# Kernel optimization log

Measured on AMD Instinct MI355X. Metric: run time of the kernel, lower is better.

The kernel has to match this reference:

```python
import jax, jax.numpy as jnp
import numpy as np

B, T, H, NH = 16, 2048, 1024, 16
HD = H // NH  # 64
IN0, IN1 = 256, 512  # modality input sizes needing projection; modality 2 is already H


def _ln(x, g, b, eps=1e-5):
    m = jnp.mean(x, axis=-1, keepdims=True)
    v = jnp.mean((x - m) ** 2, axis=-1, keepdims=True)
    return (x - m) / jnp.sqrt(v + eps) * g + b


def setup_inputs() -> dict:
    key = jax.random.key(0)
    ks = jax.random.split(key, 24)
    s = 0.02
    d = {
        'x0': jax.random.normal(ks[0], (B, T, IN0), jnp.float32),
        'x1': jax.random.normal(ks[1], (B, T, IN1), jnp.float32),
        'x2': jax.random.normal(ks[2], (B, T, H), jnp.float32),
        'static_context': jax.random.normal(ks[3], (B, T, H), jnp.float32),
        'Wp0': jax.random.normal(ks[4], (H, IN0), jnp.float32) * s,
        'bp0': jnp.zeros((H,), jnp.float32),
        'Wp1': jax.random.normal(ks[5], (H, IN1), jnp.float32) * s,
        'bp1': jnp.zeros((H,), jnp.float32),
        'Wq': jax.random.normal(ks[6], (H, H), jnp.float32) * s,
        'bq': jnp.zeros((H,), jnp.float32),
        'Wk': jax.random.normal(ks[7], (H, H), jnp.float32) * s,
        'bk': jnp.zeros((H,), jnp.float32),
        'Wv': jax.random.normal(ks[8], (H, H), jnp.float32) * s,
        'bv': jnp.zeros((H,), jnp.float32),
        'Wo': jax.random.normal(ks[9], (H, H), jnp.float32) * s,
        'bo': jnp.zeros((H,), jnp.float32),
        'query_token': jax.random.normal(ks[10], (H,), jnp.float32) * s,
        'g1': jnp.ones((H,), jnp.float32),
        'be1': jnp.zeros((H,), jnp.float32),
        'g2': jnp.ones((H,), jnp.float32),
        'be2': jnp.zeros((H,), jnp.float32),
        'W1': jax.random.normal(ks[11], (4 * H, H), jnp.float32) * s,
        'b1': jnp.zeros((4 * H,), jnp.float32),
        'W2': jax.random.normal(ks[12], (H, 4 * H), jnp.float32) * s,
        'b2': jnp.zeros((H,), jnp.float32),
    }
    return d


def _forward(x0, x1, x2, static_context, Wp0, bp0, Wp1, bp1, Wq, bq, Wk, bk, Wv, bv,
             Wo, bo, query_token, g1, be1, g2, be2, W1, b1, W2, b2):
    # project modalities to hidden size, stack -> [B, T, M, H]
    m0 = x0 @ Wp0.T + bp0
    m1 = x1 @ Wp1.T + bp1
    stacked = jnp.stack([m0, m1, x2], axis=2)  # [B,T,3,H]
    M = stacked.shape[2]
    # per-timestep single-query cross-attention over the M modality tokens,
    # batched over all B*T positions (equivalent to the torch per-t loop)
    q = query_token + static_context  # [B,T,H]
    Q = (q @ Wq.T + bq).reshape(B, T, NH, HD)
    K = (stacked @ Wk.T + bk).reshape(B, T, M, NH, HD)
    V = (stacked @ Wv.T + bv).reshape(B, T, M, NH, HD)
    scores = jnp.einsum('bthd,btmhd->bthm', Q, K) / jnp.sqrt(jnp.asarray(HD, Q.dtype))
    attn = jax.nn.softmax(scores, axis=-1)  # [B,T,NH,M]
    weights = attn.mean(axis=2)  # average over heads (torch default) -> [B,T,M]
    ctx = jnp.einsum('bthm,btmhd->bthd', attn, V).reshape(B, T, H)
    attn_out = ctx @ Wo.T + bo
    fused = _ln(attn_out, g1, be1)
    ff = jax.nn.gelu(fused @ W1.T + b1, approximate=False) @ W2.T + b2
    fused = _ln(fused + ff, g2, be2)
    return fused, weights


def reference(x0, x1, x2, static_context, Wp0, bp0, Wp1, bp1, Wq, bq, Wk, bk, Wv, bv,
              Wo, bo, query_token, g1, be1, g2, be2, W1, b1, W2, b2):
    return _forward(x0, x1, x2, static_context, Wp0, bp0, Wp1, bp1, Wq, bq, Wk, bk,
                    Wv, bv, Wo, bo, query_token, g1, be1, g2, be2, W1, b1, W2, b2)
```

## Files before the change

kernel.cpp:

```cpp
#include <hip/hip_runtime.h>
#include <hip/hip_bf16.h>
#include <math.h>

#define BT 32768
#define HH 1024

typedef unsigned short u16;
typedef __attribute__((ext_vector_type(4))) unsigned short u16x4;
typedef __attribute__((ext_vector_type(8))) __bf16 bf16x8;
typedef __attribute__((ext_vector_type(4))) float f32x4;

#define DEVI static __device__ __forceinline__

DEVI u16 f2bf(float f){
  unsigned u = __builtin_bit_cast(unsigned, f);
  u += 0x7FFFu + ((u >> 16) & 1u);
  return (u16)(u >> 16);
}
DEVI float bf2f(u16 h){
  unsigned u = ((unsigned)h) << 16;
  return __builtin_bit_cast(float, u);
}
DEVI void gl_lds16(const void* g, void* l){
  __builtin_amdgcn_global_load_lds((const __attribute__((address_space(1))) void*)g,
                                   (__attribute__((address_space(3))) void*)l, 16, 0, 0);
}
DEVI int swz(int row, int elem){ return elem ^ ((row & 7) << 3); }

__global__ void k_cast4(const float* __restrict__ s, u16* __restrict__ d, int n4){
  int i = blockIdx.x*blockDim.x + threadIdx.x;
  int st = gridDim.x*blockDim.x;
  for (; i < n4; i += st){
    float4 v = ((const float4*)s)[i];
    u16x4 o = { f2bf(v.x), f2bf(v.y), f2bf(v.z), f2bf(v.w) };
    ((u16x4*)d)[i] = o;
  }
}

__global__ void k_pack_x2(const float* __restrict__ s, u16* __restrict__ d, int n4){
  int i = blockIdx.x*blockDim.x + threadIdx.x;
  int st = gridDim.x*blockDim.x;
  for (; i < n4; i += st){
    int e = i*4; int t = e >> 10; int c = e & 1023;
    float4 v = *(const float4*)&s[e];
    u16x4 o = { f2bf(v.x), f2bf(v.y), f2bf(v.z), f2bf(v.w) };
    *(u16x4*)&d[(size_t)t*3072 + 2048 + c] = o;
  }
}

__global__ void k_qb(const float* __restrict__ qt, const float* __restrict__ sc,
                     u16* __restrict__ d, int n4){
  int i = blockIdx.x*blockDim.x + threadIdx.x;
  int st = gridDim.x*blockDim.x;
  for (; i < n4; i += st){
    int e = i*4; int c = e & 1023;
    float4 v = *(const float4*)&sc[e];
    float4 q = *(const float4*)&qt[c];
    u16x4 o = { f2bf(v.x+q.x), f2bf(v.y+q.y), f2bf(v.z+q.z), f2bf(v.w+q.w) };
    ((u16x4*)d)[i] = o;
  }
}

__global__ void k_copyf(const float* __restrict__ s, float* __restrict__ d, int n){
  int i = blockIdx.x*blockDim.x + threadIdx.x;
  int st = gridDim.x*blockDim.x;
  for (; i < n; i += st) d[i] = s[i];
}

__global__ __launch_bounds__(256, 3)
void k_gemm(const u16* __restrict__ A, int lda,
            const u16* __restrict__ B, int ldb, int K,
            const float* __restrict__ bias,
            u16* __restrict__ C, int ldc, int col0, int act)
{
  __shared__ u16 As[128*64];
  __shared__ u16 Bs[128*64];
  const int tid = threadIdx.x, lane = tid & 63, wid = tid >> 6;
  const int wr = wid >> 1, wc = wid & 1;
  const int r15 = lane & 15, g = lane >> 4;
  const int m0 = blockIdx.x * 128, n0 = blockIdx.y * 128;
  f32x4 acc[4][4] = {};

  for (int k0 = 0; k0 < K; k0 += 64){
    #pragma unroll
    for (int it = 0; it < 4; ++it){
      int c = it*256 + tid;
      int row = c >> 3;
      int ke = swz(row, (c & 7) * 8);
      gl_lds16(A + (size_t)(m0+row)*lda + (k0+ke), As + c*8);
      gl_lds16(B + (size_t)(n0+row)*ldb + (k0+ke), Bs + c*8);
    }
    __syncthreads();
    #pragma unroll
    for (int kk = 0; kk < 64; kk += 32){
      bf16x8 av[4], bvv[4];
      #pragma unroll
      for (int i = 0; i < 4; ++i){
        int row = wr*64 + i*16 + r15;
        av[i] = *(const bf16x8*)&As[row*64 + swz(row, kk + g*8)];
      }
      #pragma unroll
      for (int j = 0; j < 4; ++j){
        int row = wc*64 + j*16 + r15;
        bvv[j] = *(const bf16x8*)&Bs[row*64 + swz(row, kk + g*8)];
      }
      #pragma unroll
      for (int i = 0; i < 4; ++i)
        #pragma unroll
        for (int j = 0; j < 4; ++j)
          acc[i][j] = __builtin_amdgcn_mfma_f32_16x16x32_bf16(av[i], bvv[j], acc[i][j], 0, 0, 0);
    }
    __syncthreads();
  }
  #pragma unroll
  for (int j = 0; j < 4; ++j){
    int col = wc*64 + j*16 + r15;
    float bb = bias ? bias[n0 + col] : 0.f;
    #pragma unroll
    for (int i = 0; i < 4; ++i){
      #pragma unroll
      for (int jj = 0; jj < 4; ++jj){
        int row = wr*64 + i*16 + g*4 + jj;
        float v = acc[i][j][jj] + bb;
        if (act == 1) v = 0.5f * v * (1.f + erff(v * 0.70710678118654752f));
        C[(size_t)(m0+row)*ldc + col0 + n0 + col] = f2bf(v);
      }
    }
  }
}

__global__ __launch_bounds__(256, 3)
void k_attn(const u16* __restrict__ S, const u16* __restrict__ Wk, const u16* __restrict__ Wv,
            const float* __restrict__ bk, const float* __restrict__ bv,
            const u16* __restrict__ Q, u16* __restrict__ ctx, float* __restrict__ wacc)
{
  __shared__ __align__(16) char smem[45056];
  u16* As  = (u16*)smem;
  u16* Bk  = (u16*)(smem + 12288);
  u16* Bv  = (u16*)(smem + 12288 + 16384);
  u16* Vl  = (u16*)smem;
  u16* Ql  = (u16*)(smem + 24576);
  float* Sl = (float*)(smem + 24576 + 8192);

  const int tid = threadIdx.x, lane = tid & 63, wid = tid >> 6;
  const int wr = wid >> 1, wcH = wid & 1;
  const int r15 = lane & 15, g = lane >> 4;
  const int bt = blockIdx.x, bn = blockIdx.y;
  const int row0 = bt * 96, n0 = bn * 128;

  f32x4 aK[3][4] = {}; f32x4 aV[3][4] = {};

  for (int k0 = 0; k0 < 1024; k0 += 64){
    #pragma unroll
    for (int it = 0; it < 3; ++it){
      int c = it*256 + tid; int row = c >> 3;
      int ke = swz(row, (c & 7) * 8);
      gl_lds16(S + (size_t)(row0+row)*1024 + k0 + ke, As + c*8);
    }
    #pragma unroll
    for (int it = 0; it < 4; ++it){
      int c = it*256 + tid; int row = c >> 3;
      int ke = swz(row, (c & 7) * 8);
      gl_lds16(Wk + (size_t)(n0+row)*1024 + k0 + ke, Bk + c*8);
      gl_lds16(Wv + (size_t)(n0+row)*1024 + k0 + ke, Bv + c*8);
    }
    __syncthreads();
    #pragma unroll
    for (int kk = 0; kk < 64; kk += 32){
      bf16x8 av[3], b1[4], b2[4];
      #pragma unroll
      for (int i = 0; i < 3; ++i){
        int row = wr*48 + i*16 + r15;
        av[i] = *(const bf16x8*)&As[row*64 + swz(row, kk + g*8)];
      }
      #pragma unroll
      for (int j = 0; j < 4; ++j){
        int row = wcH*64 + j*16 + r15;
        b1[j] = *(const bf16x8*)&Bk[row*64 + swz(row, kk + g*8)];
        b2[j] = *(const bf16x8*)&Bv[row*64 + swz(row, kk + g*8)];
      }
      #pragma unroll
      for (int i = 0; i < 3; ++i)
        #pragma unroll
        for (int j = 0; j < 4; ++j){
          aK[i][j] = __builtin_amdgcn_mfma_f32_16x16x32_bf16(av[i], b1[j], aK[i][j], 0, 0, 0);
          aV[i][j] = __builtin_amdgcn_mfma_f32_16x16x32_bf16(av[i], b2[j], aV[i][j], 0, 0, 0);
        }
    }
    __syncthreads();
  }

  #pragma unroll
  for (int j = 0; j < 4; ++j){
    int col = wcH*64 + j*16 + r15;
    float bvv = bv[n0 + col];
    #pragma unroll
    for (int i = 0; i < 3; ++i)
      #pragma unroll
      for (int jj = 0; jj < 4; ++jj){
        int row = wr*48 + i*16 + g*4 + jj;
        Vl[row*128 + col] = f2bf(aV[i][j][jj] + bvv);
      }
  }
  #pragma unroll
  for (int it = 0; it < 4; ++it){
    int c4 = it*256 + tid;
    int tt = c4 >> 5, cc = (c4 & 31)*4;
    *(u16x4*)&Ql[tt*128 + cc] = *(const u16x4*)&Q[(size_t)(bt*32 + tt)*1024 + n0 + cc];
  }
  __syncthreads();

  float bkv[4];
  #pragma unroll
  for (int j = 0; j < 4; ++j) bkv[j] = bk[n0 + wcH*64 + j*16 + r15];
  #pragma unroll
  for (int i = 0; i < 3; ++i){
    #pragma unroll
    for (int jj = 0; jj < 4; ++jj){
      int row = wr*48 + i*16 + g*4 + jj;
      int tt = row / 3;
      float s = 0.f;
      #pragma unroll
      for (int j = 0; j < 4; ++j){
        float qv = bf2f(Ql[tt*128 + wcH*64 + j*16 + r15]);
        s += (aK[i][j][jj] + bkv[j]) * qv;
      }
      s += __shfl_xor(s, 1); s += __shfl_xor(s, 2);
      s += __shfl_xor(s, 4); s += __shfl_xor(s, 8);
      if (r15 == 0) Sl[wcH*96 + row] = s * 0.125f;
    }
  }
  __syncthreads();

  const int t0 = bt*32;
  #pragma unroll
  for (int it = 0; it < 16; ++it){
    int idx = it*256 + tid;
    int tt = idx >> 7, col = idx & 127;
    int h = col >> 6;
    float s0 = Sl[h*96 + tt*3 + 0];
    float s1 = Sl[h*96 + tt*3 + 1];
    float s2 = Sl[h*96 + tt*3 + 2];
    float mx = fmaxf(s0, fmaxf(s1, s2));
    float e0 = expf(s0-mx), e1 = expf(s1-mx), e2 = expf(s2-mx);
    float inv = 1.f/(e0+e1+e2);
    e0 *= inv; e1 *= inv; e2 *= inv;
    float c = e0*bf2f(Vl[(tt*3+0)*128 + col])
            + e1*bf2f(Vl[(tt*3+1)*128 + col])
            + e2*bf2f(Vl[(tt*3+2)*128 + col]);
    ctx[(size_t)(t0+tt)*1024 + n0 + col] = f2bf(c);
    if ((col & 63) == 0){
      atomicAdd(&wacc[(size_t)(t0+tt)*3 + 0], e0*0.0625f);
      atomicAdd(&wacc[(size_t)(t0+tt)*3 + 1], e1*0.0625f);
      atomicAdd(&wacc[(size_t)(t0+tt)*3 + 2], e2*0.0625f);
    }
  }
}

__global__ __launch_bounds__(256)
void k_ln(const u16* __restrict__ X, const u16* __restrict__ R,
          const float* __restrict__ gam, const float* __restrict__ bet,
          u16* __restrict__ outb, float* __restrict__ outf)
{
  __shared__ float rs[4], rq[4];
  const int t = blockIdx.x, tid = threadIdx.x;
  const size_t base = (size_t)t*1024 + tid*4;
  u16x4 xv = *(const u16x4*)&X[base];
  float v[4];
  #pragma unroll
  for (int i = 0; i < 4; ++i) v[i] = bf2f(xv[i]);
  if (R){
    u16x4 rv = *(const u16x4*)&R[base];
    #pragma unroll
    for (int i = 0; i < 4; ++i) v[i] += bf2f(rv[i]);
  }
  float s = v[0]+v[1]+v[2]+v[3];
  float q = v[0]*v[0]+v[1]*v[1]+v[2]*v[2]+v[3]*v[3];
  #pragma unroll
  for (int m = 1; m < 64; m <<= 1){ s += __shfl_xor(s, m); q += __shfl_xor(q, m); }
  if ((tid & 63) == 0){ rs[tid>>6] = s; rq[tid>>6] = q; }
  __syncthreads();
  s = rs[0]+rs[1]+rs[2]+rs[3];
  q = rq[0]+rq[1]+rq[2]+rq[3];
  float mean = s * (1.f/1024.f);
  float var  = q * (1.f/1024.f) - mean*mean;
  float rstd = rsqrtf(var + 1e-5f);
  int c0 = tid*4;
  if (outb){
    u16x4 o;
    #pragma unroll
    for (int i = 0; i < 4; ++i) o[i] = f2bf((v[i]-mean)*rstd*gam[c0+i] + bet[c0+i]);
    *(u16x4*)&outb[base] = o;
  } else {
    float4 o;
    o.x = (v[0]-mean)*rstd*gam[c0+0] + bet[c0+0];
    o.y = (v[1]-mean)*rstd*gam[c0+1] + bet[c0+1];
    o.z = (v[2]-mean)*rstd*gam[c0+2] + bet[c0+2];
    o.w = (v[3]-mean)*rstd*gam[c0+3] + bet[c0+3];
    *(float4*)&outf[base] = o;
  }
}

extern "C" void kernel_launch(void* const* d_in, const int* in_sizes, int n_in,
                              void* d_out, int out_size, void* d_ws, size_t ws_size,
                              hipStream_t stream)
{
  (void)in_sizes; (void)n_in; (void)out_size;
  const float* x0  = (const float*)d_in[0];
  const float* x1  = (const float*)d_in[1];
  const float* x2  = (const float*)d_in[2];
  const float* sc  = (const float*)d_in[3];
  const float* Wp0 = (const float*)d_in[4];  const float* bp0 = (const float*)d_in[5];
  const float* Wp1 = (const float*)d_in[6];  const float* bp1 = (const float*)d_in[7];
  const float* Wq  = (const float*)d_in[8];  const float* bq  = (const float*)d_in[9];
  const float* Wk  = (const float*)d_in[10]; const float* bk  = (const float*)d_in[11];
  const float* Wv  = (const float*)d_in[12]; const float* bv  = (const float*)d_in[13];
  const float* Wo  = (const float*)d_in[14]; const float* bo  = (const float*)d_in[15];
  const float* qt  = (const float*)d_in[16];
  const float* g1  = (const float*)d_in[17]; const float* be1 = (const float*)d_in[18];
  const float* g2  = (const float*)d_in[19]; const float* be2 = (const float*)d_in[20];
  const float* W1  = (const float*)d_in[21]; const float* b1  = (const float*)d_in[22];
  const float* W2  = (const float*)d_in[23]; const float* b2  = (const float*)d_in[24];

  char* ws = (char*)d_ws;
  size_t off = 0;
  auto alloc = [&](size_t b)->char*{ char* p = ws + off; off += (b + 255) & ~(size_t)255; return p; };

  u16* Wp0b = (u16*)alloc((size_t)1024*256*2);
  u16* Wp1b = (u16*)alloc((size_t)1024*512*2);
  u16* Wqb  = (u16*)alloc((size_t)1024*1024*2);
  u16* Wkb  = (u16*)alloc((size_t)1024*1024*2);
  u16* Wvb  = (u16*)alloc((size_t)1024*1024*2);
  u16* Wob  = (u16*)alloc((size_t)1024*1024*2);
  u16* W1b  = (u16*)alloc((size_t)4096*1024*2);
  u16* W2b  = (u16*)alloc((size_t)1024*4096*2);
  char* stackedR = alloc((size_t)3*BT*1024*2);
  char* regA = alloc((size_t)BT*1024*2);
  char* regB = alloc((size_t)BT*1024*2);
  float* wacc = (float*)alloc((size_t)BT*3*4);
  if (off > ws_size) return;

  u16* stackedb = (u16*)stackedR;
  u16* ff1c = (u16*)stackedR;
  u16* x0b = (u16*)regA;
  u16* x1b = (u16*)(regA + (size_t)BT*256*2);
  u16* Qb  = (u16*)regA;
  u16* aob = (u16*)regA;
  u16* ff2b = (u16*)regA;
  u16* qb  = (u16*)regB;
  u16* ctxb = (u16*)regB;
  u16* f1b = (u16*)regB;

  hipMemsetAsync(wacc, 0, (size_t)BT*3*4, stream);

  dim3 B256(256);
  auto cast4 = [&](const float* s, u16* d, int n){
    k_cast4<<<dim3(1024), B256, 0, stream>>>(s, d, n >> 2);
  };
  cast4(Wp0, Wp0b, 1024*256); cast4(Wp1, Wp1b, 1024*512);
  cast4(Wq, Wqb, 1024*1024);  cast4(Wk, Wkb, 1024*1024);
  cast4(Wv, Wvb, 1024*1024);  cast4(Wo, Wob, 1024*1024);
  cast4(W1, W1b, 4096*1024);  cast4(W2, W2b, 4096*1024);
  cast4(x0, x0b, BT*256);     cast4(x1, x1b, BT*512);
  k_pack_x2<<<dim3(2048), B256, 0, stream>>>(x2, stackedb, BT*256);
  k_qb<<<dim3(2048), B256, 0, stream>>>(qt, sc, qb, BT*256);

  k_gemm<<<dim3(BT/128, 8), B256, 0, stream>>>(x0b, 256, Wp0b, 256, 256, bp0, stackedb, 3072, 0,    0);
  k_gemm<<<dim3(BT/128, 8), B256, 0, stream>>>(x1b, 512, Wp1b, 512, 512, bp1, stackedb, 3072, 1024, 0);
  k_gemm<<<dim3(BT/128, 8), B256, 0, stream>>>(qb, 1024, Wqb, 1024, 1024, bq, Qb, 1024, 0, 0);
  k_attn<<<dim3(BT/32, 8), B256, 0, stream>>>(stackedb, Wkb, Wvb, bk, bv, Qb, ctxb, wacc);
  k_gemm<<<dim3(BT/128, 8), B256, 0, stream>>>(ctxb, 1024, Wob, 1024, 1024, bo, aob, 1024, 0, 0);
  k_ln<<<dim3(BT), B256, 0, stream>>>(aob, nullptr, g1, be1, f1b, nullptr);

  for (int c = 0; c < 4; ++c){
    const u16* fa = f1b + (size_t)c*8192*1024;
    k_gemm<<<dim3(64, 32), B256, 0, stream>>>(fa, 1024, W1b, 1024, 1024, b1, ff1c, 4096, 0, 1);
    k_gemm<<<dim3(64, 8),  B256, 0, stream>>>(ff1c, 4096, W2b, 4096, 4096, b2,
                                              ff2b + (size_t)c*8192*1024, 1024, 0, 0);
  }
  float* outf = (float*)d_out;
  k_ln<<<dim3(BT), B256, 0, stream>>>(ff2b, f1b, g2, be2, nullptr, outf);
  k_copyf<<<dim3(384), B256, 0, stream>>>(wacc, outf + (size_t)BT*1024, BT*3);
}
```

Measured before the change: 1.704 ms.

## Use 256x256 double-buffered GEMM tiles with 512 threads and reorder attention grid

Replaces the 128x128 single-buffered GEMM with a 256x256 tile kernel using 8 waves, double-buffered LDS and prefetch of the next K-slice issued before computing the current one, with MFMA sections raised to higher priority. The goal is more data reuse per LDS load and overlap of global loads with matrix math. The attention launch grid is transposed so that blocks sharing the same row tile are scheduled adjacently, which should improve cache reuse of the stacked activations. In exchange, the larger tiles need 128KB of LDS and many accumulator registers, which lowers occupancy and leaves fewer blocks per wave for the smaller GEMMs.

```diff
diff --git a/kernel.cpp b/kernel.cpp
--- a/kernel.cpp
+++ b/kernel.cpp
@@ -67,60 +67,90 @@
   for (; i < n; i += st) d[i] = s[i];
 }
 
-__global__ __launch_bounds__(256, 3)
-void k_gemm(const u16* __restrict__ A, int lda,
-            const u16* __restrict__ B, int ldb, int K,
-            const float* __restrict__ bias,
-            u16* __restrict__ C, int ldc, int col0, int act)
+__global__ __launch_bounds__(512, 2)
+void k_gemm256(const u16* __restrict__ A, int lda,
+               const u16* __restrict__ B, int ldb, int K,
+               const float* __restrict__ bias,
+               u16* __restrict__ C, int ldc, int col0, int act)
 {
-  __shared__ u16 As[128*64];
-  __shared__ u16 Bs[128*64];
-  const int tid = threadIdx.x, lane = tid & 63, wid = tid >> 6;
-  const int wr = wid >> 1, wc = wid & 1;
+  __shared__ u16 As[2][256*64];
+  __shared__ u16 Bs[2][256*64];
+  const int tid = threadIdx.x, lane = tid & 63;
+  const int wid = tid >> 6;
+  const int wr = wid >> 2, wc = wid & 3;
   const int r15 = lane & 15, g = lane >> 4;
-  const int m0 = blockIdx.x * 128, n0 = blockIdx.y * 128;
-  f32x4 acc[4][4] = {};
-
-  for (int k0 = 0; k0 < K; k0 += 64){
-    #pragma unroll
-    for (int it = 0; it < 4; ++it){
-      int c = it*256 + tid;
-      int row = c >> 3;
-      int ke = swz(row, (c & 7) * 8);
-      gl_lds16(A + (size_t)(m0+row)*lda + (k0+ke), As + c*8);
-      gl_lds16(B + (size_t)(n0+row)*ldb + (k0+ke), Bs + c*8);
-    }
-    __syncthreads();
+  const int m0 = blockIdx.x * 256, n0 = blockIdx.y * 256;
+  f32x4 acc[8][4] = {};
+
+  const int srow = tid >> 3;
+  const int scol = (tid & 7) * 8;
+
+  auto stage = [&](int t, int b){
+    const int k0 = t * 64;
+    #pragma unroll
+    for (int r = 0; r < 4; ++r){
+      int row = r*64 + srow;
+      int ke = swz(row, scol);
+      gl_lds16(A + (size_t)(m0+row)*lda + (k0+ke), &As[b][row*64 + scol]);
+    }
+    #pragma unroll
+    for (int r = 0; r < 4; ++r){
+      int row = r*64 + srow;
+      int ke = swz(row, scol);
+      gl_lds16(B + (size_t)(n0+row)*ldb + (k0+ke), &Bs[b][row*64 + scol]);
+    }
+  };
+
+  auto compute = [&](int b){
+    __builtin_amdgcn_s_setprio(1);
     #pragma unroll
     for (int kk = 0; kk < 64; kk += 32){
-      bf16x8 av[4], bvv[4];
-      #pragma unroll
-      for (int i = 0; i < 4; ++i){
-        int row = wr*64 + i*16 + r15;
-        av[i] = *(const bf16x8*)&As[row*64 + swz(row, kk + g*8)];
+      bf16x8 av[8], bv[4];
+      #pragma unroll
+      for (int i = 0; i < 8; ++i){
+        int row = wr*128 + i*16 + r15;
+        av[i] = *(const bf16x8*)&As[b][row*64 + swz(row, kk + g*8)];
       }
       #pragma unroll
       for (int j = 0; j < 4; ++j){
         int row = wc*64 + j*16 + r15;
-        bvv[j] = *(const bf16x8*)&Bs[row*64 + swz(row, kk + g*8)];
-      }
-      #pragma unroll
-      for (int i = 0; i < 4; ++i)
+        bv[j] = *(const bf16x8*)&Bs[b][row*64 + swz(row, kk + g*8)];
+      }
+      #pragma unroll
+      for (int i = 0; i < 8; ++i)
         #pragma unroll
         for (int j = 0; j < 4; ++j)
-          acc[i][j] = __builtin_amdgcn_mfma_f32_16x16x32_bf16(av[i], bvv[j], acc[i][j], 0, 0, 0);
-    }
-    __syncthreads();
-  }
+          acc[i][j] = __builtin_amdgcn_mfma_f32_16x16x32_bf16(av[i], bv[j], acc[i][j], 0, 0, 0);
+    }
+    __builtin_amdgcn_s_setprio(0);
+  };
+
+  const int nt = K >> 6;
+  stage(0, 0);
+  for (int t = 0; t < nt-1; ++t){
+    stage(t+1, (t+1)&1);
+    asm volatile("s_waitcnt vmcnt(8)" ::: "memory");
+    __builtin_amdgcn_s_barrier();
+    asm volatile("" ::: "memory");
+    compute(t&1);
+    asm volatile("" ::: "memory");
+    __builtin_amdgcn_s_barrier();
+    asm volatile("" ::: "memory");
+  }
+  asm volatile("s_waitcnt vmcnt(0)" ::: "memory");
+  __builtin_amdgcn_s_barrier();
+  asm volatile("" ::: "memory");
+  compute((nt-1)&1);
+
   #pragma unroll
   for (int j = 0; j < 4; ++j){
     int col = wc*64 + j*16 + r15;
     float bb = bias ? bias[n0 + col] : 0.f;
     #pragma unroll
-    for (int i = 0; i < 4; ++i){
+    for (int i = 0; i < 8; ++i){
       #pragma unroll
       for (int jj = 0; jj < 4; ++jj){
-        int row = wr*64 + i*16 + g*4 + jj;
+        int row = wr*128 + i*16 + g*4 + jj;
         float v = acc[i][j][jj] + bb;
         if (act == 1) v = 0.5f * v * (1.f + erff(v * 0.70710678118654752f));
         C[(size_t)(m0+row)*ldc + col0 + n0 + col] = f2bf(v);
@@ -145,7 +175,7 @@
   const int tid = threadIdx.x, lane = tid & 63, wid = tid >> 6;
   const int wr = wid >> 1, wcH = wid & 1;
   const int r15 = lane & 15, g = lane >> 4;
-  const int bt = blockIdx.x, bn = blockIdx.y;
+  const int bn = blockIdx.x, bt = blockIdx.y;
   const int row0 = bt * 96, n0 = bn * 128;
 
   f32x4 aK[3][4] = {}; f32x4 aV[3][4] = {};
@@ -353,7 +383,7 @@
 
   hipMemsetAsync(wacc, 0, (size_t)BT*3*4, stream);
 
-  dim3 B256(256);
+  dim3 B256(256), B512(512);
   auto cast4 = [&](const float* s, u16* d, int n){
     k_cast4<<<dim3(1024), B256, 0, stream>>>(s, d, n >> 2);
   };
@@ -365,18 +395,18 @@
   k_pack_x2<<<dim3(2048), B256, 0, stream>>>(x2, stackedb, BT*256);
   k_qb<<<dim3(2048), B256, 0, stream>>>(qt, sc, qb, BT*256);
 
-  k_gemm<<<dim3(BT/128, 8), B256, 0, stream>>>(x0b, 256, Wp0b, 256, 256, bp0, stackedb, 3072, 0,    0);
-  k_gemm<<<dim3(BT/128, 8), B256, 0, stream>>>(x1b, 512, Wp1b, 512, 512, bp1, stackedb, 3072, 1024, 0);
-  k_gemm<<<dim3(BT/128, 8), B256, 0, stream>>>(qb, 1024, Wqb, 1024, 1024, bq, Qb, 1024, 0, 0);
-  k_attn<<<dim3(BT/32, 8), B256, 0, stream>>>(stackedb, Wkb, Wvb, bk, bv, Qb, ctxb, wacc);
-  k_gemm<<<dim3(BT/128, 8), B256, 0, stream>>>(ctxb, 1024, Wob, 1024, 1024, bo, aob, 1024, 0, 0);
+  k_gemm256<<<dim3(BT/256, 4), B512, 0, stream>>>(x0b, 256, Wp0b, 256, 256, bp0, stackedb, 3072, 0,    0);
+  k_gemm256<<<dim3(BT/256, 4), B512, 0, stream>>>(x1b, 512, Wp1b, 512, 512, bp1, stackedb, 3072, 1024, 0);
+  k_gemm256<<<dim3(BT/256, 4), B512, 0, stream>>>(qb, 1024, Wqb, 1024, 1024, bq, Qb, 1024, 0, 0);
+  k_attn<<<dim3(8, BT/32), B256, 0, stream>>>(stackedb, Wkb, Wvb, bk, bv, Qb, ctxb, wacc);
+  k_gemm256<<<dim3(BT/256, 4), B512, 0, stream>>>(ctxb, 1024, Wob, 1024, 1024, bo, aob, 1024, 0, 0);
   k_ln<<<dim3(BT), B256, 0, stream>>>(aob, nullptr, g1, be1, f1b, nullptr);
 
   for (int c = 0; c < 4; ++c){
     const u16* fa = f1b + (size_t)c*8192*1024;
-    k_gemm<<<dim3(64, 32), B256, 0, stream>>>(fa, 1024, W1b, 1024, 1024, b1, ff1c, 4096, 0, 1);
-    k_gemm<<<dim3(64, 8),  B256, 0, stream>>>(ff1c, 4096, W2b, 4096, 4096, b2,
-                                              ff2b + (size_t)c*8192*1024, 1024, 0, 0);
+    k_gemm256<<<dim3(32, 16), B512, 0, stream>>>(fa, 1024, W1b, 1024, 1024, b1, ff1c, 4096, 0, 1);
+    k_gemm256<<<dim3(32, 4),  B512, 0, stream>>>(ff1c, 4096, W2b, 4096, 4096, b2,
+                                                 ff2b + (size_t)c*8192*1024, 1024, 0, 0);
   }
   float* outf = (float*)d_out;
   k_ln<<<dim3(BT), B256, 0, stream>>>(ff2b, f1b, g2, be2, nullptr, outf);
```

Result: slower. 2.075 ms (+21.8%).

## Fold modality projections into K/V weights and fuse projection into attention

Applied to the files above, without the earlier changes.

Precomputes combined weights Wk·Wp0 and Wk·Wp1 (and the V counterparts) plus folded biases, so K and V are computed straight from the raw modality inputs with K=256/512 instead of first materialising the projected stacked tensor. This removes the two projection GEMMs and the large stacked buffer write and read. The attention kernel is restructured into two passes per tile: a scores pass over all modalities, then a V pass accumulating softmax-weighted context. The price is extra small weight-prep GEMMs and a change in rounding, since the folded weights are stored in bf16.

```diff
diff --git a/kernel.cpp b/kernel.cpp
--- a/kernel.cpp
+++ b/kernel.cpp
@@ -34,17 +34,6 @@
     float4 v = ((const float4*)s)[i];
     u16x4 o = { f2bf(v.x), f2bf(v.y), f2bf(v.z), f2bf(v.w) };
     ((u16x4*)d)[i] = o;
-  }
-}
-
-__global__ void k_pack_x2(const float* __restrict__ s, u16* __restrict__ d, int n4){
-  int i = blockIdx.x*blockDim.x + threadIdx.x;
-  int st = gridDim.x*blockDim.x;
-  for (; i < n4; i += st){
-    int e = i*4; int t = e >> 10; int c = e & 1023;
-    float4 v = *(const float4*)&s[e];
-    u16x4 o = { f2bf(v.x), f2bf(v.y), f2bf(v.z), f2bf(v.w) };
-    *(u16x4*)&d[(size_t)t*3072 + 2048 + c] = o;
   }
 }
 
@@ -65,6 +54,28 @@
   int i = blockIdx.x*blockDim.x + threadIdx.x;
   int st = gridDim.x*blockDim.x;
   for (; i < n; i += st) d[i] = s[i];
+}
+
+__global__ void k_transcast(const float* __restrict__ s, u16* __restrict__ d, int R, int C){
+  __shared__ float tile[32][33];
+  int c0 = blockIdx.x*32, r0 = blockIdx.y*32;
+  int tx = threadIdx.x & 31, ty = threadIdx.x >> 5;
+  #pragma unroll
+  for (int i = 0; i < 32; i += 8) tile[ty+i][tx] = s[(size_t)(r0+ty+i)*C + c0+tx];
+  __syncthreads();
+  #pragma unroll
+  for (int i = 0; i < 32; i += 8) d[(size_t)(c0+ty+i)*R + r0+tx] = f2bf(tile[tx][ty+i]);
+}
+
+__global__ void k_matvec(const u16* __restrict__ W, const float* __restrict__ x,
+                         const float* __restrict__ badd, float* __restrict__ out, int K){
+  int row = blockIdx.x*4 + (threadIdx.x>>6);
+  int lane = threadIdx.x & 63;
+  float s = 0.f;
+  for (int k = lane; k < K; k += 64) s += bf2f(W[(size_t)row*K + k]) * x[k];
+  #pragma unroll
+  for (int m = 1; m < 64; m <<= 1) s += __shfl_xor(s, m);
+  if (lane == 0) out[row] = s + badd[row];
 }
 
 __global__ __launch_bounds__(256, 3)
@@ -129,130 +140,161 @@
   }
 }
 
-__global__ __launch_bounds__(256, 3)
-void k_attn(const u16* __restrict__ S, const u16* __restrict__ Wk, const u16* __restrict__ Wv,
-            const float* __restrict__ bk, const float* __restrict__ bv,
-            const u16* __restrict__ Q, u16* __restrict__ ctx, float* __restrict__ wacc)
+__global__ __launch_bounds__(512, 4)
+void k_attn2p(const u16* __restrict__ x0b, const u16* __restrict__ x1b, const u16* __restrict__ x2b,
+              const u16* __restrict__ Wc0, const u16* __restrict__ Wc1, const u16* __restrict__ Wc2,
+              const float* __restrict__ bc0, const float* __restrict__ bc1, const float* __restrict__ bc2,
+              const u16* __restrict__ Qg, u16* __restrict__ ctx, float* __restrict__ wacc)
 {
-  __shared__ __align__(16) char smem[45056];
-  u16* As  = (u16*)smem;
-  u16* Bk  = (u16*)(smem + 12288);
-  u16* Bv  = (u16*)(smem + 12288 + 16384);
-  u16* Vl  = (u16*)smem;
-  u16* Ql  = (u16*)(smem + 24576);
-  float* Sl = (float*)(smem + 24576 + 8192);
+  __shared__ __align__(16) u16 As[128*64];
+  __shared__ __align__(16) u16 Bs[128*64];
+  __shared__ float Sl[2*128*3];
 
   const int tid = threadIdx.x, lane = tid & 63, wid = tid >> 6;
-  const int wr = wid >> 1, wcH = wid & 1;
+  const int wr = wid >> 1, h = wid & 1;
   const int r15 = lane & 15, g = lane >> 4;
-  const int bt = blockIdx.x, bn = blockIdx.y;
-  const int row0 = bt * 96, n0 = bn * 128;
-
-  f32x4 aK[3][4] = {}; f32x4 aV[3][4] = {};
-
-  for (int k0 = 0; k0 < 1024; k0 += 64){
-    #pragma unroll
-    for (int it = 0; it < 3; ++it){
-      int c = it*256 + tid; int row = c >> 3;
-      int ke = swz(row, (c & 7) * 8);
-      gl_lds16(S + (size_t)(row0+row)*1024 + k0 + ke, As + c*8);
-    }
-    #pragma unroll
-    for (int it = 0; it < 4; ++it){
-      int c = it*256 + tid; int row = c >> 3;
-      int ke = swz(row, (c & 7) * 8);
-      gl_lds16(Wk + (size_t)(n0+row)*1024 + k0 + ke, Bk + c*8);
-      gl_lds16(Wv + (size_t)(n0+row)*1024 + k0 + ke, Bv + c*8);
-    }
-    __syncthreads();
-    #pragma unroll
-    for (int kk = 0; kk < 64; kk += 32){
-      bf16x8 av[3], b1[4], b2[4];
-      #pragma unroll
-      for (int i = 0; i < 3; ++i){
-        int row = wr*48 + i*16 + r15;
-        av[i] = *(const bf16x8*)&As[row*64 + swz(row, kk + g*8)];
-      }
-      #pragma unroll
-      for (int j = 0; j < 4; ++j){
-        int row = wcH*64 + j*16 + r15;
-        b1[j] = *(const bf16x8*)&Bk[row*64 + swz(row, kk + g*8)];
-        b2[j] = *(const bf16x8*)&Bv[row*64 + swz(row, kk + g*8)];
-      }
-      #pragma unroll
-      for (int i = 0; i < 3; ++i)
+  const int bid = blockIdx.x;
+  const int bn = bid & 7, btb = bid >> 3;
+  const int t0 = btb * 128, n0 = bn * 128;
+
+  const u16* Xs[3] = { x0b, x1b, x2b };
+  const u16* Ws[3] = { Wc0, Wc1, Wc2 };
+  const float* Bc[3] = { bc0, bc1, bc2 };
+  const int Ks[3] = { 256, 512, 1024 };
+
+  const int srow = tid >> 3;
+  const int scol = (tid & 7) * 8;
+
+  #pragma unroll
+  for (int m = 0; m < 3; ++m){
+    const int K = Ks[m];
+    const u16* X = Xs[m];
+    const u16* W = Ws[m];
+    f32x4 aK[2][4] = {};
+    for (int k0 = 0; k0 < K; k0 += 64){
+      #pragma unroll
+      for (int l = 0; l < 2; ++l){
+        int row = l*64 + srow;
+        int ke = swz(row, scol);
+        gl_lds16(X + (size_t)(t0+row)*K + k0 + ke, &As[row*64 + scol]);
+        gl_lds16(W + (size_t)(n0+row)*K + k0 + ke, &Bs[row*64 + scol]);
+      }
+      __syncthreads();
+      #pragma unroll
+      for (int kk = 0; kk < 64; kk += 32){
+        bf16x8 av[2], bv[4];
+        #pragma unroll
+        for (int i = 0; i < 2; ++i){
+          int ra = wr*32 + i*16 + r15;
+          av[i] = *(const bf16x8*)&As[ra*64 + swz(ra, kk + g*8)];
+        }
         #pragma unroll
         for (int j = 0; j < 4; ++j){
-          aK[i][j] = __builtin_amdgcn_mfma_f32_16x16x32_bf16(av[i], b1[j], aK[i][j], 0, 0, 0);
-          aV[i][j] = __builtin_amdgcn_mfma_f32_16x16x32_bf16(av[i], b2[j], aV[i][j], 0, 0, 0);
+          int rb = h*64 + j*16 + r15;
+          bv[j] = *(const bf16x8*)&Bs[rb*64 + swz(rb, kk + g*8)];
         }
-    }
-    __syncthreads();
-  }
-
-  #pragma unroll
-  for (int j = 0; j < 4; ++j){
-    int col = wcH*64 + j*16 + r15;
-    float bvv = bv[n0 + col];
-    #pragma unroll
-    for (int i = 0; i < 3; ++i)
+        #pragma unroll
+        for (int i = 0; i < 2; ++i)
+          #pragma unroll
+          for (int j = 0; j < 4; ++j)
+            aK[i][j] = __builtin_amdgcn_mfma_f32_16x16x32_bf16(av[i], bv[j], aK[i][j], 0, 0, 0);
+      }
+      __syncthreads();
+    }
+    float bkc[4];
+    #pragma unroll
+    for (int j = 0; j < 4; ++j) bkc[j] = Bc[m][n0 + h*64 + j*16 + r15];
+    #pragma unroll
+    for (int i = 0; i < 2; ++i){
       #pragma unroll
       for (int jj = 0; jj < 4; ++jj){
-        int row = wr*48 + i*16 + g*4 + jj;
-        Vl[row*128 + col] = f2bf(aV[i][j][jj] + bvv);
-      }
-  }
-  #pragma unroll
-  for (int it = 0; it < 4; ++it){
-    int c4 = it*256 + tid;
-    int tt = c4 >> 5, cc = (c4 & 31)*4;
-    *(u16x4*)&Ql[tt*128 + cc] = *(const u16x4*)&Q[(size_t)(bt*32 + tt)*1024 + n0 + cc];
+        int tt = wr*32 + i*16 + g*4 + jj;
+        const u16* qrow = Qg + (size_t)(t0+tt)*1024 + n0 + h*64 + r15;
+        float s = 0.f;
+        #pragma unroll
+        for (int j = 0; j < 4; ++j)
+          s += (aK[i][j][jj] + bkc[j]) * bf2f(qrow[j*16]);
+        s += __shfl_xor(s, 1); s += __shfl_xor(s, 2);
+        s += __shfl_xor(s, 4); s += __shfl_xor(s, 8);
+        if (r15 == 0) Sl[(h*128 + tt)*3 + m] = s * 0.125f;
+      }
+    }
   }
   __syncthreads();
-
-  float bkv[4];
-  #pragma unroll
-  for (int j = 0; j < 4; ++j) bkv[j] = bk[n0 + wcH*64 + j*16 + r15];
-  #pragma unroll
-  for (int i = 0; i < 3; ++i){
-    #pragma unroll
-    for (int jj = 0; jj < 4; ++jj){
-      int row = wr*48 + i*16 + g*4 + jj;
-      int tt = row / 3;
-      float s = 0.f;
-      #pragma unroll
-      for (int j = 0; j < 4; ++j){
-        float qv = bf2f(Ql[tt*128 + wcH*64 + j*16 + r15]);
-        s += (aK[i][j][jj] + bkv[j]) * qv;
-      }
-      s += __shfl_xor(s, 1); s += __shfl_xor(s, 2);
-      s += __shfl_xor(s, 4); s += __shfl_xor(s, 8);
-      if (r15 == 0) Sl[wcH*96 + row] = s * 0.125f;
-    }
-  }
-  __syncthreads();
-
-  const int t0 = bt*32;
-  #pragma unroll
-  for (int it = 0; it < 16; ++it){
-    int idx = it*256 + tid;
-    int tt = idx >> 7, col = idx & 127;
-    int h = col >> 6;
-    float s0 = Sl[h*96 + tt*3 + 0];
-    float s1 = Sl[h*96 + tt*3 + 1];
-    float s2 = Sl[h*96 + tt*3 + 2];
+  if (tid < 256){
+    int h2 = tid >> 7, tt = tid & 127;
+    int base = (h2*128 + tt)*3;
+    float s0 = Sl[base+0], s1 = Sl[base+1], s2 = Sl[base+2];
     float mx = fmaxf(s0, fmaxf(s1, s2));
     float e0 = expf(s0-mx), e1 = expf(s1-mx), e2 = expf(s2-mx);
     float inv = 1.f/(e0+e1+e2);
     e0 *= inv; e1 *= inv; e2 *= inv;
-    float c = e0*bf2f(Vl[(tt*3+0)*128 + col])
-            + e1*bf2f(Vl[(tt*3+1)*128 + col])
-            + e2*bf2f(Vl[(tt*3+2)*128 + col]);
-    ctx[(size_t)(t0+tt)*1024 + n0 + col] = f2bf(c);
-    if ((col & 63) == 0){
-      atomicAdd(&wacc[(size_t)(t0+tt)*3 + 0], e0*0.0625f);
-      atomicAdd(&wacc[(size_t)(t0+tt)*3 + 1], e1*0.0625f);
-      atomicAdd(&wacc[(size_t)(t0+tt)*3 + 2], e2*0.0625f);
+    Sl[base+0] = e0; Sl[base+1] = e1; Sl[base+2] = e2;
+    atomicAdd(&wacc[(size_t)(t0+tt)*3 + 0], e0*0.0625f);
+    atomicAdd(&wacc[(size_t)(t0+tt)*3 + 1], e1*0.0625f);
+    atomicAdd(&wacc[(size_t)(t0+tt)*3 + 2], e2*0.0625f);
+  }
+  __syncthreads();
+
+  f32x4 ctxa[2][4] = {};
+  #pragma unroll
+  for (int m = 0; m < 3; ++m){
+    const int K = Ks[m];
+    const u16* X = Xs[m];
+    const u16* W = Ws[m] + (size_t)1024*K;
+    f32x4 aV[2][4] = {};
+    for (int k0 = 0; k0 < K; k0 += 64){
+      #pragma unroll
+      for (int l = 0; l < 2; ++l){
+        int row = l*64 + srow;
+        int ke = swz(row, scol);
+        gl_lds16(X + (size_t)(t0+row)*K + k0 + ke, &As[row*64 + scol]);
+        gl_lds16(W + (size_t)(n0+row)*K + k0 + ke, &Bs[row*64 + scol]);
+      }
+      __syncthreads();
+      #pragma unroll
+      for (int kk = 0; kk < 64; kk += 32){
+        bf16x8 av[2], bv[4];
+        #pragma unroll
+        for (int i = 0; i < 2; ++i){
+          int ra = wr*32 + i*16 + r15;
+          av[i] = *(const bf16x8*)&As[ra*64 + swz(ra, kk + g*8)];
+        }
+        #pragma unroll
+        for (int j = 0; j < 4; ++j){
+          int rb = h*64 + j*16 + r15;
+          bv[j] = *(const bf16x8*)&Bs[rb*64 + swz(rb, kk + g*8)];
+        }
+        #pragma unroll
+        for (int i = 0; i < 2; ++i)
+          #pragma unroll
+          for (int j = 0; j < 4; ++j)
+            aV[i][j] = __builtin_amdgcn_mfma_f32_16x16x32_bf16(av[i], bv[j], aV[i][j], 0, 0, 0);
+      }
+      __syncthreads();
+    }
+    #pragma unroll
+    for (int j = 0; j < 4; ++j){
+      float bvv = Bc[m][1024 + n0 + h*64 + j*16 + r15];
+      #pragma unroll
+      for (int i = 0; i < 2; ++i){
+        #pragma unroll
+        for (int jj = 0; jj < 4; ++jj){
+          int tt = wr*32 + i*16 + g*4 + jj;
+          float p = Sl[(h*128 + tt)*3 + m];
+          ctxa[i][j][jj] += p * (aV[i][j][jj] + bvv);
+        }
+      }
+    }
+  }
+  #pragma unroll
+  for (int i = 0; i < 2; ++i){
+    #pragma unroll
+    for (int jj = 0; jj < 4; ++jj){
+      int tt = wr*32 + i*16 + g*4 + jj;
+      #pragma unroll
+      for (int j = 0; j < 4; ++j)
+        ctx[(size_t)(t0+tt)*1024 + n0 + h*64 + j*16 + r15] = f2bf(ctxa[i][j][jj]);
     }
   }
 }
@@ -326,49 +368,64 @@
   size_t off = 0;
   auto alloc = [&](size_t b)->char*{ char* p = ws + off; off += (b + 255) & ~(size_t)255; return p; };
 
-  u16* Wp0b = (u16*)alloc((size_t)1024*256*2);
-  u16* Wp1b = (u16*)alloc((size_t)1024*512*2);
-  u16* Wqb  = (u16*)alloc((size_t)1024*1024*2);
-  u16* Wkb  = (u16*)alloc((size_t)1024*1024*2);
-  u16* Wvb  = (u16*)alloc((size_t)1024*1024*2);
-  u16* Wob  = (u16*)alloc((size_t)1024*1024*2);
-  u16* W1b  = (u16*)alloc((size_t)4096*1024*2);
-  u16* W2b  = (u16*)alloc((size_t)1024*4096*2);
-  char* stackedR = alloc((size_t)3*BT*1024*2);
-  char* regA = alloc((size_t)BT*1024*2);
-  char* regB = alloc((size_t)BT*1024*2);
+  u16* Wqb   = (u16*)alloc((size_t)1024*1024*2);
+  u16* Wob   = (u16*)alloc((size_t)1024*1024*2);
+  u16* W1b   = (u16*)alloc((size_t)4096*1024*2);
+  u16* W2b   = (u16*)alloc((size_t)1024*4096*2);
+  u16* Wkvb  = (u16*)alloc((size_t)2048*1024*2);
+  u16* Wp0t  = (u16*)alloc((size_t)256*1024*2);
+  u16* Wp1t  = (u16*)alloc((size_t)512*1024*2);
+  u16* Wkv0c = (u16*)alloc((size_t)2048*256*2);
+  u16* Wkv1c = (u16*)alloc((size_t)2048*512*2);
+  float* bc0 = (float*)alloc((size_t)2048*4);
+  float* bc1 = (float*)alloc((size_t)2048*4);
+  float* bc2 = (float*)alloc((size_t)2048*4);
+  char* regX  = alloc((size_t)BT*(256+512+1024)*2);
+  char* regQ1 = alloc((size_t)BT*1024*2);
+  char* regQ2 = alloc((size_t)BT*1024*2);
   float* wacc = (float*)alloc((size_t)BT*3*4);
   if (off > ws_size) return;
 
-  u16* stackedb = (u16*)stackedR;
-  u16* ff1c = (u16*)stackedR;
-  u16* x0b = (u16*)regA;
-  u16* x1b = (u16*)(regA + (size_t)BT*256*2);
-  u16* Qb  = (u16*)regA;
-  u16* aob = (u16*)regA;
-  u16* ff2b = (u16*)regA;
-  u16* qb  = (u16*)regB;
-  u16* ctxb = (u16*)regB;
-  u16* f1b = (u16*)regB;
+  u16* x0b = (u16*)regX;
+  u16* x1b = (u16*)(regX + (size_t)BT*256*2);
+  u16* x2b = (u16*)(regX + (size_t)BT*768*2);
+  u16* aob  = (u16*)regX;
+  u16* ff2b = (u16*)regX;
+  u16* qb   = (u16*)regQ1;
+  u16* ctxb = (u16*)regQ1;
+  u16* f1b  = (u16*)regQ1;
+  u16* Qb   = (u16*)regQ2;
+  u16* ff1c = (u16*)regQ2;
 
   hipMemsetAsync(wacc, 0, (size_t)BT*3*4, stream);
 
-  dim3 B256(256);
-  auto cast4 = [&](const float* s, u16* d, int n){
-    k_cast4<<<dim3(1024), B256, 0, stream>>>(s, d, n >> 2);
+  dim3 B256(256), B512(512);
+  auto cast4 = [&](const float* s, u16* d, int n, int grid){
+    k_cast4<<<dim3(grid), B256, 0, stream>>>(s, d, n >> 2);
   };
-  cast4(Wp0, Wp0b, 1024*256); cast4(Wp1, Wp1b, 1024*512);
-  cast4(Wq, Wqb, 1024*1024);  cast4(Wk, Wkb, 1024*1024);
-  cast4(Wv, Wvb, 1024*1024);  cast4(Wo, Wob, 1024*1024);
-  cast4(W1, W1b, 4096*1024);  cast4(W2, W2b, 4096*1024);
-  cast4(x0, x0b, BT*256);     cast4(x1, x1b, BT*512);
-  k_pack_x2<<<dim3(2048), B256, 0, stream>>>(x2, stackedb, BT*256);
+  cast4(Wq, Wqb, 1024*1024, 1024);
+  cast4(Wk, Wkvb, 1024*1024, 1024);
+  cast4(Wv, Wkvb + (size_t)1024*1024, 1024*1024, 1024);
+  cast4(Wo, Wob, 1024*1024, 1024);
+  cast4(W1, W1b, 4096*1024, 1024);
+  cast4(W2, W2b, 4096*1024, 1024);
+  cast4(x0, x0b, BT*256, 1024);
+  cast4(x1, x1b, BT*512, 1024);
+  cast4(x2, x2b, BT*1024, 2048);
+  k_transcast<<<dim3(8, 32),  B256, 0, stream>>>(Wp0, Wp0t, 1024, 256);
+  k_transcast<<<dim3(16, 32), B256, 0, stream>>>(Wp1, Wp1t, 1024, 512);
+  k_copyf<<<dim3(4), B256, 0, stream>>>(bk, bc2, 1024);
+  k_copyf<<<dim3(4), B256, 0, stream>>>(bv, bc2 + 1024, 1024);
+  k_matvec<<<dim3(512), B256, 0, stream>>>(Wkvb, bp0, bc2, bc0, 1024);
+  k_matvec<<<dim3(512), B256, 0, stream>>>(Wkvb, bp1, bc2, bc1, 1024);
   k_qb<<<dim3(2048), B256, 0, stream>>>(qt, sc, qb, BT*256);
 
-  k_gemm<<<dim3(BT/128, 8), B256, 0, stream>>>(x0b, 256, Wp0b, 256, 256, bp0, stackedb, 3072, 0,    0);
-  k_gemm<<<dim3(BT/128, 8), B256, 0, stream>>>(x1b, 512, Wp1b, 512, 512, bp1, stackedb, 3072, 1024, 0);
+  k_gemm<<<dim3(16, 2), B256, 0, stream>>>(Wkvb, 1024, Wp0t, 1024, 1024, nullptr, Wkv0c, 256, 0, 0);
+  k_gemm<<<dim3(16, 4), B256, 0, stream>>>(Wkvb, 1024, Wp1t, 1024, 1024, nullptr, Wkv1c, 512, 0, 0);
+
   k_gemm<<<dim3(BT/128, 8), B256, 0, stream>>>(qb, 1024, Wqb, 1024, 1024, bq, Qb, 1024, 0, 0);
-  k_attn<<<dim3(BT/32, 8), B256, 0, stream>>>(stackedb, Wkb, Wvb, bk, bv, Qb, ctxb, wacc);
+  k_attn2p<<<dim3(BT/128*8), B512, 0, stream>>>(x0b, x1b, x2b, Wkv0c, Wkv1c, Wkvb,
+                                                bc0, bc1, bc2, Qb, ctxb, wacc);
   k_gemm<<<dim3(BT/128, 8), B256, 0, stream>>>(ctxb, 1024, Wob, 1024, 1024, bo, aob, 1024, 0, 0);
   k_ln<<<dim3(BT), B256, 0, stream>>>(aob, nullptr, g1, be1, f1b, nullptr);
 
```

Result: faster. 1.591 ms (-6.6%).
